# Performance work log

Hardware: AMD Instinct MI355X
Metric: run time of the kernel (lower is better)

Reference implementation:

```python
import jax, jax.numpy as jnp
import numpy as np

I, H, NH, A = 128, 2048, 2, 4   # input_size, hidden_size, n_hidden, alpha_dim
K = 2 * A * A                   # per-position theta entries
B = 8192


def make_masks():
    # MADE sequential-ordering masks, identical to DART.create_masks
    inp = np.arange(I)
    degrees = [inp] + [np.arange(H) % (I - 1) for _ in range(NH + 1)] + [np.arange(I) - 1]
    masks = [(d1[:, None] >= d0[None, :]).astype(np.float32)
             for d0, d1 in zip(degrees[:-1], degrees[1:])]
    # last mask repeated per theta entry: repeat(1, K).view(-1, H) == row-repeat
    masks[-1] = np.repeat(masks[-1], K, axis=0)
    return [jnp.asarray(m) for m in masks]


def setup_inputs() -> dict:
    key = jax.random.key(0)
    ks = jax.random.split(key, 5)
    x = jax.random.normal(ks[0], (B, I), dtype=jnp.float32)

    def lin(k, out_dim, in_dim):
        kw, kb = jax.random.split(k)
        s = 1.0 / np.sqrt(in_dim)
        W = jax.random.uniform(kw, (out_dim, in_dim), minval=-s, maxval=s, dtype=jnp.float32)
        b = jax.random.uniform(kb, (out_dim,), minval=-s, maxval=s, dtype=jnp.float32)
        return W, b

    W0, b0 = lin(ks[1], H, I)
    W1, b1 = lin(ks[2], H, H)
    W2, b2 = lin(ks[3], H, H)
    W3, b3 = lin(ks[4], I * K, H)
    return dict(x=x, W0=W0, b0=b0, W1=W1, b1=b1, W2=W2, b2=b2, W3=W3, b3=b3)


def logexpmm(a, b):
    # log-domain matmul: out[..., i, j] = logsumexp_k(a[..., i, k] + b[..., k, j])
    return jax.nn.logsumexp(a[..., :, :, None] + b[..., None, :, :], axis=-2)


def reference(x, W0, b0, W1, b1, W2, b2, W3, b3):
    m = make_masks()
    h = jax.nn.relu(x @ (m[0] * W0).T + b0)
    h = jax.nn.relu(h @ (m[1] * W1).T + b1)
    h = jax.nn.relu(h @ (m[2] * W2).T + b2)
    theta = (h @ (m[3] * W3).T + b3).reshape(-1, I, 2, A, A)
    mu, alpha = theta[:, :, 0], theta[:, :, 1]  # (B, I, A, A)

    LOG2PI = float(np.log(2.0 * np.pi))
    xe = x[:, :, None, None]
    # Normal(mu, exp(alpha)).log_prob(x) - log(alpha_dim)
    logp = (-0.5 * ((xe - mu) * jnp.exp(-alpha)) ** 2
            - alpha - 0.5 * LOG2PI - jnp.log(jnp.float32(A)))

    first = logp[:, 0, 0:1]        # (B, 1, A)
    last = logp[:, -1, :, 0:1]     # (B, A, 1)
    inner = jnp.swapaxes(logp[:, 1:-1], 0, 1)  # (I-2, B, A, A)

    def step(carry, mtx):
        return logexpmm(carry, mtx), None

    prod, _ = jax.lax.scan(step, inner[0], inner[1:])
    return logexpmm(first, logexpmm(prod, last))  # (B, 1, 1)
```

## Files before the change

### kernel.cpp

```cpp
#include <hip/hip_runtime.h>
#include <hip/hip_bf16.h>
#include <cstdint>
#include <cstddef>

#define AS1 __attribute__((address_space(1)))
#define AS3 __attribute__((address_space(3)))

typedef __bf16 bf16x8  __attribute__((ext_vector_type(8)));
typedef float  floatx4 __attribute__((ext_vector_type(4)));

__device__ __forceinline__ void load_lds16(const void* g, void* l) {
    __builtin_amdgcn_global_load_lds((AS1 void*)g, (AS3 void*)l, 16, 0, 0);
}

__device__ __forceinline__ float fexp2(float x) { return __builtin_amdgcn_exp2f(x); }
__device__ __forceinline__ float flog2(float x) { return __builtin_amdgcn_logf(x); }

#define LOG2E 1.4426950408889634f
#define LN2   0.6931471805599453f
#define C0K   2.3052328943245633f

__device__ __forceinline__ float logp2(float xv, float mu, float al) {
    float e = fexp2(-al * LOG2E);
    float z = (xv - mu) * e;
    return (-0.5f * z * z - al - C0K) * LOG2E;
}
__device__ __forceinline__ float lse4(float a0, float a1, float a2, float a3) {
    float mx = fmaxf(fmaxf(a0, a1), fmaxf(a2, a3));
    return mx + flog2(fexp2(a0 - mx) + fexp2(a1 - mx) +
                      fexp2(a2 - mx) + fexp2(a3 - mx));
}
__device__ __forceinline__ void lmm4(const float* Aa, const float* Bb, float* D) {
#pragma unroll
    for (int r = 0; r < 4; ++r)
#pragma unroll
        for (int c = 0; c < 4; ++c)
            D[r * 4 + c] = lse4(Aa[r * 4 + 0] + Bb[0 * 4 + c],
                                Aa[r * 4 + 1] + Bb[1 * 4 + c],
                                Aa[r * 4 + 2] + Bb[2 * 4 + c],
                                Aa[r * 4 + 3] + Bb[3 * 4 + c]);
}

__device__ __forceinline__ int resp_s(int p) {
    return p < 272 ? p / 17 : 16 + ((p - 272) >> 4);
}
__device__ __forceinline__ int invp_s(int p) {
    if (p < 272) { int d = p / 17; int r = p - d * 17;
                   return r < 16 ? d + r * 127 : 2032 + d; }
    int d = 16 + ((p - 272) >> 4); int j = (p - 272) & 15;
    return d + j * 127;
}
__device__ __forceinline__ int cnt_le(int D) {
    return D < 16 ? (D + 1) * 17 : 272 + ((D - 15) << 4);
}

__global__ __launch_bounds__(256)
void prep_all(const float* __restrict__ x,  const float* __restrict__ W0,
              const float* __restrict__ W1, const float* __restrict__ W2,
              const float* __restrict__ W3,
              __bf16* __restrict__ xb,  __bf16* __restrict__ w0m,
              __bf16* __restrict__ w1m, __bf16* __restrict__ w2m,
              __bf16* __restrict__ w3m)
{
    __shared__ float lds[2048];
    const int blk = blockIdx.x;
    const int tid = threadIdx.x;
    const int t8  = tid * 8;

    if (blk < 640) {
        bf16x8 o;
        if (blk < 512) {
            size_t base = (size_t)blk * 2048 + t8;
            floatx4 a = *(const floatx4*)(x + base);
            floatx4 b = *(const floatx4*)(x + base + 4);
#pragma unroll
            for (int j = 0; j < 4; ++j) { o[j] = (__bf16)a[j]; o[4 + j] = (__bf16)b[j]; }
            *(bf16x8*)(xb + base) = o;
        } else {
            long idx = (long)(blk - 512) * 2048 + t8;
            int p_n = (int)(idx >> 7);
            int c   = (int)(idx & 127);
            int dg  = resp_s(p_n);
            const float* s = W0 + (long)invp_s(p_n) * 128 + c;
            floatx4 a = *(const floatx4*)s;
            floatx4 b = *(const floatx4*)(s + 4);
#pragma unroll
            for (int j = 0; j < 8; ++j) {
                float v = j < 4 ? a[j] : b[j - 4];
                o[j] = (__bf16)((dg >= c + j) ? v : 0.0f);
            }
            *(bf16x8*)(w0m + idx) = o;
        }
        return;
    }

    const float* srow; __bf16* drow; int deg_n; bool strict;
    if (blk < 2688) {
        int p_n = blk - 640;
        srow = W1 + (size_t)invp_s(p_n) * 2048; drow = w1m + (size_t)p_n * 2048;
        deg_n = resp_s(p_n); strict = false;
    } else if (blk < 4736) {
        int p_n = blk - 2688;
        srow = W2 + (size_t)invp_s(p_n) * 2048; drow = w2m + (size_t)p_n * 2048;
        deg_n = resp_s(p_n); strict = false;
    } else {
        int n = blk - 4736;
        srow = W3 + (size_t)n * 2048; drow = w3m + (size_t)n * 2048;
        deg_n = n >> 5; strict = true;
    }
    floatx4 a = *(const floatx4*)(srow + t8);
    floatx4 b = *(const floatx4*)(srow + t8 + 4);
    *(floatx4*)&lds[t8]     = a;
    *(floatx4*)&lds[t8 + 4] = b;
    __syncthreads();
    bf16x8 o;
#pragma unroll
    for (int j = 0; j < 8; ++j) {
        int p = t8 + j;
        float v = lds[invp_s(p)];
        int dg = resp_s(p);
        bool keep = strict ? (deg_n > dg) : (deg_n >= dg);
        o[j] = (__bf16)(keep ? v : 0.0f);
    }
    *(bf16x8*)(drow + t8) = o;
}

template <bool RELU, bool OBF16, bool TLAYOUT, bool PERMBIAS, int LMODE>
__global__ __launch_bounds__(256, 4)
void gemm_bt(const __bf16* __restrict__ A, const __bf16* __restrict__ Bw,
             const float* __restrict__ bias, void* __restrict__ Cout,
             int N, int K)
{
    __shared__ __align__(16) __bf16 lsA[128 * 64];
    __shared__ __align__(16) __bf16 lsB[128 * 64];
    const int tid  = threadIdx.x;
    const int wave = tid >> 6;
    const int lane = tid & 63;
    const int bm = blockIdx.x;
    const int bn = (gridDim.y - 1) - blockIdx.y;
    const int wm = wave >> 1, wn = wave & 1;

    const int r8 = lane >> 3;
    const int cb = (lane & 7) ^ r8;
    const __bf16* gsrc[8];
    __bf16* ldst[8];
#pragma unroll
    for (int t = 0; t < 8; ++t) {
        int j = wave * 8 + t;
        if (j < 16) {
            int row = bm * 128 + j * 8 + r8;
            gsrc[t] = A + (size_t)row * K + cb * 8;
            ldst[t] = lsA + j * 512;
        } else {
            int jj = j - 16;
            int row = bn * 128 + jj * 8 + r8;
            gsrc[t] = Bw + (size_t)row * K + cb * 8;
            ldst[t] = lsB + jj * 512;
        }
    }

    const int fr  = lane & 15;
    const int ks  = lane >> 4;
    const int sx  = fr & 7;
    const int sl0 = ((ks)     ^ sx) * 8;
    const int sl1 = ((4 + ks) ^ sx) * 8;
    const __bf16* arow[4];
    const __bf16* brow[4];
#pragma unroll
    for (int i = 0; i < 4; ++i) {
        arow[i] = lsA + (wm * 64 + i * 16 + fr) * 64;
        brow[i] = lsB + (wn * 64 + i * 16 + fr) * 64;
    }

    floatx4 acc[4][4];
    const floatx4 vzero = {0.f, 0.f, 0.f, 0.f};
#pragma unroll
    for (int mi = 0; mi < 4; ++mi)
#pragma unroll
        for (int ni = 0; ni < 4; ++ni) acc[mi][ni] = vzero;

    const int nk = K >> 6;
    int limit;
    if (LMODE == 0)      limit = (cnt_le(resp_s(bn * 128 + 127)) + 63) >> 6;
    else if (LMODE == 1) { int D = 4 * bn + 2; if (D > 126) D = 126;
                           limit = (cnt_le(D) + 63) >> 6; }
    else                 limit = (resp_s(bn * 128 + 127) + 64) >> 6;
    if (limit > nk) limit = nk;

    for (int it = 0; it < limit; ++it) {
        const int kt = it << 6;
        __syncthreads();
#pragma unroll
        for (int t = 0; t < 8; ++t)
            load_lds16((const void*)(gsrc[t] + kt), (void*)ldst[t]);
        __syncthreads();
        bf16x8 af[4], bf[4];
#pragma unroll
        for (int i = 0; i < 4; ++i) af[i] = *(const bf16x8*)(arow[i] + sl0);
#pragma unroll
        for (int i = 0; i < 4; ++i) bf[i] = *(const bf16x8*)(brow[i] + sl0);
#pragma unroll
        for (int mi = 0; mi < 4; ++mi)
#pragma unroll
            for (int ni = 0; ni < 4; ++ni)
                acc[mi][ni] = __builtin_amdgcn_mfma_f32_16x16x32_bf16(
                    af[mi], bf[ni], acc[mi][ni], 0, 0, 0);
#pragma unroll
        for (int i = 0; i < 4; ++i) af[i] = *(const bf16x8*)(arow[i] + sl1);
#pragma unroll
        for (int i = 0; i < 4; ++i) bf[i] = *(const bf16x8*)(brow[i] + sl1);
#pragma unroll
        for (int mi = 0; mi < 4; ++mi)
#pragma unroll
            for (int ni = 0; ni < 4; ++ni)
                acc[mi][ni] = __builtin_amdgcn_mfma_f32_16x16x32_bf16(
                    af[mi], bf[ni], acc[mi][ni], 0, 0, 0);
    }

    const int cn  = lane & 15;
    const int cr4 = (lane >> 4) * 4;
#pragma unroll
    for (int ni = 0; ni < 4; ++ni) {
        int col = bn * 128 + wn * 64 + ni * 16 + cn;
        float bv = bias[PERMBIAS ? invp_s(col) : col];
#pragma unroll
        for (int mi = 0; mi < 4; ++mi) {
            int row0 = bm * 128 + wm * 64 + mi * 16 + cr4;
#pragma unroll
            for (int q = 0; q < 4; ++q) {
                float v = acc[mi][ni][q] + bv;
                if (RELU) v = fmaxf(v, 0.f);
                if (TLAYOUT) {
                    size_t addr = (size_t)(bm * 2 + wm) * ((size_t)N * 64)
                                + (size_t)(col >> 5) * 2048
                                + (size_t)(mi * 16 + cr4 + q) * 32 + (col & 31);
                    ((__bf16*)Cout)[addr] = (__bf16)v;
                } else if (OBF16) {
                    ((__bf16*)Cout)[(size_t)(row0 + q) * N + col] = (__bf16)v;
                } else {
                    ((float*)Cout)[(size_t)(row0 + q) * N + col] = v;
                }
            }
        }
    }
}

#define CFENCE() asm volatile("" ::: "memory")
#define BARX()  do { CFENCE(); __builtin_amdgcn_s_barrier(); CFENCE(); } while (0)
#define WVM2()  asm volatile("s_waitcnt vmcnt(2)" ::: "memory")
#define WVM0()  asm volatile("s_waitcnt vmcnt(0)" ::: "memory")
#define WLGK()  asm volatile("s_waitcnt lgkmcnt(0)" ::: "memory")

template <bool RELU, bool OBF16, bool TLAYOUT, bool PERMBIAS, int LMODE>
__global__ __launch_bounds__(512)
void gemm8p(const __bf16* __restrict__ A, const __bf16* __restrict__ Bw,
            const float* __restrict__ bias, void* __restrict__ Cout,
            int N, int K)
{
    __shared__ __align__(16) __bf16 ls[2 * 24576];
    const int tid  = threadIdx.x;
    const int wave = tid >> 6;
    const int lane = tid & 63;
    const int bm = blockIdx.x;
    const int bn = (gridDim.y - 1) - blockIdx.y;
    const int wm = wave >> 1, wn = wave & 1;

    const int l8 = lane >> 3;
    const int cb = (lane & 7) ^ l8;
    const __bf16* gA[2][2];  int dA[2][2];
    const __bf16* gB[2];     int dB[2];
#pragma unroll
    for (int h = 0; h < 2; ++h)
#pragma unroll
        for (int s = 0; s < 2; ++s) {
            int rt = h * 128 + wave * 16 + s * 8;
            gA[h][s] = A + (size_t)(bm * 256 + rt + l8) * K + cb * 8;
            dA[h][s] = rt * 64;
        }
#pragma unroll
    for (int s = 0; s < 2; ++s) {
        int rt = wave * 16 + s * 8;
        gB[s] = Bw + (size_t)(bn * 128 + rt + l8) * K + cb * 8;
        dB[s] = 16384 + rt * 64;
    }

#define STG_A(buf, kt) do { \
    load_lds16((const void*)(gA[0][0] + (kt)), (void*)(ls + (buf)*24576 + dA[0][0])); \
    load_lds16((const void*)(gA[0][1] + (kt)), (void*)(ls + (buf)*24576 + dA[0][1])); \
    load_lds16((const void*)(gA[1][0] + (kt)), (void*)(ls + (buf)*24576 + dA[1][0])); \
    load_lds16((const void*)(gA[1][1] + (kt)), (void*)(ls + (buf)*24576 + dA[1][1])); } while (0)
#define STG_B(buf, kt) do { \
    load_lds16((const void*)(gB[0] + (kt)), (void*)(ls + (buf)*24576 + dB[0])); \
    load_lds16((const void*)(gB[1] + (kt)), (void*)(ls + (buf)*24576 + dB[1])); } while (0)

    const int fr  = lane & 15;
    const int ks  = lane >> 4;
    const int sx  = fr & 7;
    const int sl0 = ((ks)     ^ sx) * 8;
    const int sl1 = ((4 + ks) ^ sx) * 8;
    int aoff[4], boff[4];
#pragma unroll
    for (int i = 0; i < 4; ++i) {
        aoff[i] = (wm * 64 + i * 16 + fr) * 64;
        boff[i] = 16384 + (wn * 64 + i * 16 + fr) * 64;
    }

    floatx4 acc[4][4];
    const floatx4 vzero = {0.f, 0.f, 0.f, 0.f};
#pragma unroll
    for (int mi = 0; mi < 4; ++mi)
#pragma unroll
        for (int ni = 0; ni < 4; ++ni) acc[mi][ni] = vzero;

    bf16x8 bfr[4][2], afr[2][2];

#define DSRD_B(buf) do { \
    _Pragma("unroll") \
    for (int ni = 0; ni < 4; ++ni) { \
        bfr[ni][0] = *(const bf16x8*)(ls + (buf)*24576 + boff[ni] + sl0); \
        bfr[ni][1] = *(const bf16x8*)(ls + (buf)*24576 + boff[ni] + sl1); } } while (0)
#define DSRD_A(buf, q) do { \
    _Pragma("unroll") \
    for (int j = 0; j < 2; ++j) { \
        afr[j][0] = *(const bf16x8*)(ls + (buf)*24576 + aoff[2*(q)+j] + sl0); \
        afr[j][1] = *(const bf16x8*)(ls + (buf)*24576 + aoff[2*(q)+j] + sl1); } } while (0)
#define MFMA16(q) do { \
    __builtin_amdgcn_s_setprio(1); \
    _Pragma("unroll") \
    for (int j = 0; j < 2; ++j) \
    _Pragma("unroll") \
    for (int ni = 0; ni < 4; ++ni) { \
        acc[2*(q)+j][ni] = __builtin_amdgcn_mfma_f32_16x16x32_bf16( \
            afr[j][0], bfr[ni][0], acc[2*(q)+j][ni], 0, 0, 0); \
        acc[2*(q)+j][ni] = __builtin_amdgcn_mfma_f32_16x16x32_bf16( \
            afr[j][1], bfr[ni][1], acc[2*(q)+j][ni], 0, 0, 0); } \
    __builtin_amdgcn_s_setprio(0); } while (0)

    const int nk = K >> 6;
    int limit;
    if (LMODE == 0)      limit = (cnt_le(resp_s(bn * 128 + 127)) + 63) >> 6;
    else if (LMODE == 1) { int D = 4 * bn + 2; if (D > 126) D = 126;
                           limit = (cnt_le(D) + 63) >> 6; }
    else                 limit = (resp_s(bn * 128 + 127) + 64) >> 6;
    if (limit > nk) limit = nk;
    const int NT = limit;

    STG_B(0, 0);
    STG_A(0, 0);
    if (NT > 1) { STG_B(1, 64); WVM2(); } else { WVM0(); }
    BARX();

    for (int t = 0; ; t += 2) {
        const int kt1 = (t + 1) << 6, kt2 = (t + 2) << 6, kt3 = (t + 3) << 6;
        const bool has1 = t + 1 < NT, has2 = t + 2 < NT, has3 = t + 3 < NT;

        DSRD_B(0);
        DSRD_A(0, 0);
        if (has1) STG_A(1, kt1);
        BARX(); WLGK();
        MFMA16(0);
        BARX();

        DSRD_A(0, 1);
        if (has2) STG_B(0, kt2);
        BARX(); WLGK();
        MFMA16(1);
        if (!has1) break;
        if (has2) WVM2(); else WVM0();
        BARX();

        DSRD_B(1);
        DSRD_A(1, 0);
        if (has2) STG_A(0, kt2);
        BARX(); WLGK();
        MFMA16(0);
        BARX();

        DSRD_A(1, 1);
        if (has3) STG_B(1, kt3);
        BARX(); WLGK();
        MFMA16(1);
        if (!has2) break;
        if (has3) WVM2(); else WVM0();
        BARX();
    }

    const int cn  = lane & 15;
    const int cr4 = (lane >> 4) * 4;
#pragma unroll
    for (int ni = 0; ni < 4; ++ni) {
        int col = bn * 128 + wn * 64 + ni * 16 + cn;
        float bv = bias[PERMBIAS ? invp_s(col) : col];
#pragma unroll
        for (int mi = 0; mi < 4; ++mi) {
            int row0 = bm * 256 + wm * 64 + mi * 16 + cr4;
#pragma unroll
            for (int q = 0; q < 4; ++q) {
                float v = acc[mi][ni][q] + bv;
                if (RELU) v = fmaxf(v, 0.f);
                if (TLAYOUT) {
                    size_t addr = (size_t)(bm * 4 + wm) * ((size_t)N * 64)
                                + (size_t)(col >> 5) * 2048
                                + (size_t)(mi * 16 + cr4 + q) * 32 + (col & 31);
                    ((__bf16*)Cout)[addr] = (__bf16)v;
                } else if (OBF16) {
                    ((__bf16*)Cout)[(size_t)(row0 + q) * N + col] = (__bf16)v;
                } else {
                    ((float*)Cout)[(size_t)(row0 + q) * N + col] = v;
                }
            }
        }
    }
#undef STG_A
#undef STG_B
#undef DSRD_B
#undef DSRD_A
#undef MFMA16
}

__global__ __launch_bounds__(576)
void chain_all(const __bf16* __restrict__ th2,
               const float* __restrict__ x,
               float* __restrict__ out)
{
    __shared__ float xs[32 * 129];
    __shared__ float Pl[32 * 306];
    const int tid = threadIdx.x;
    const int blk = blockIdx.x;

    for (int idx = tid; idx < 4096; idx += 576) {
        int bl = idx >> 7, i = idx & 127;
        xs[bl * 129 + i] = x[(size_t)blk * 4096 + idx];
    }
    __syncthreads();

    const int s  = tid >> 5;
    const int bl = tid & 31;
    const int b64 = (blk & 1) * 32 + bl;
    const __bf16* tb = th2 + (size_t)(blk >> 1) * 262144 + (size_t)b64 * 32;

    {
        const int i0 = 1 + s * 7;
        const __bf16* tp = tb + (size_t)i0 * 2048;
        float M[4][4];
#pragma unroll
        for (int r = 0; r < 4; ++r)
#pragma unroll
            for (int c = 0; c < 4; ++c) M[r][c] = (r == c) ? 0.f : -1e30f;

        for (int ii = 0; ii < 7; ++ii) {
            bf16x8 v0 = *(const bf16x8*)(tp);
            bf16x8 v1 = *(const bf16x8*)(tp + 8);
            bf16x8 v2 = *(const bf16x8*)(tp + 16);
            bf16x8 v3 = *(const bf16x8*)(tp + 24);
            float mu[16], al[16];
#pragma unroll
            for (int j = 0; j < 8; ++j) {
                mu[j] = (float)v0[j]; mu[8 + j] = (float)v1[j];
                al[j] = (float)v2[j]; al[8 + j] = (float)v3[j];
            }
            float xv = xs[bl * 129 + i0 + ii];
            tp += 2048;
            float lp[16];
#pragma unroll
            for (int j = 0; j < 16; ++j) lp[j] = logp2(xv, mu[j], al[j]);
            float Mn[4][4];
#pragma unroll
            for (int r = 0; r < 4; ++r)
#pragma unroll
                for (int c = 0; c < 4; ++c)
                    Mn[r][c] = lse4(M[r][0] + lp[0 + c], M[r][1] + lp[4 + c],
                                    M[r][2] + lp[8 + c], M[r][3] + lp[12 + c]);
#pragma unroll
            for (int r = 0; r < 4; ++r)
#pragma unroll
                for (int c = 0; c < 4; ++c) M[r][c] = Mn[r][c];
        }
        float* pb = Pl + bl * 306 + s * 17;
#pragma unroll
        for (int r = 0; r < 4; ++r)
#pragma unroll
            for (int c = 0; c < 4; ++c) pb[r * 4 + c] = M[r][c];
    }
    __syncthreads();

    float Q[16];
    if (tid < 288) {
        const float* base = Pl + bl * 306;
        lmm4(base + (2 * s) * 17, base + (2 * s + 1) * 17, Q);
    }
    __syncthreads();
    if (tid < 288) {
        float* dst = Pl + bl * 306 + s * 17;
#pragma unroll
        for (int e = 0; e < 16; ++e) dst[e] = Q[e];
    }
    __syncthreads();

    if (tid < 32) {
        const float* base = Pl + tid * 306;
        float M[16], T[16];
#pragma unroll
        for (int e = 0; e < 16; ++e) M[e] = base[e];
#pragma unroll
        for (int j = 1; j < 9; ++j) {
            lmm4(M, base + j * 17, T);
#pragma unroll
            for (int e = 0; e < 16; ++e) M[e] = T[e];
        }
        const int bb64 = (blk & 1) * 32 + tid;
        const __bf16* tbb = th2 + (size_t)(blk >> 1) * 262144 + (size_t)bb64 * 32;
        float x0 = xs[tid * 129 + 0];
        float xl = xs[tid * 129 + 127];
        float last[4], t4[4], f4[4];
#pragma unroll
        for (int c = 0; c < 4; ++c)
            last[c] = logp2(xl, (float)tbb[(size_t)127 * 2048 + c * 4],
                                (float)tbb[(size_t)127 * 2048 + 16 + c * 4]);
#pragma unroll
        for (int r = 0; r < 4; ++r)
            t4[r] = lse4(M[r * 4 + 0] + last[0], M[r * 4 + 1] + last[1],
                         M[r * 4 + 2] + last[2], M[r * 4 + 3] + last[3]);
#pragma unroll
        for (int r = 0; r < 4; ++r)
            f4[r] = logp2(x0, (float)tbb[r], (float)tbb[16 + r]);
        out[blk * 32 + tid] = LN2 * lse4(f4[0] + t4[0], f4[1] + t4[1],
                                         f4[2] + t4[2], f4[3] + t4[3]);
    }
}

extern "C" void kernel_launch(void* const* d_in, const int* in_sizes, int n_in,
                              void* d_out, int out_size, void* d_ws, size_t ws_size,
                              hipStream_t stream)
{
    (void)in_sizes; (void)n_in; (void)out_size; (void)ws_size;
    const float* x  = (const float*)d_in[0];
    const float* W0 = (const float*)d_in[1];
    const float* b0 = (const float*)d_in[2];
    const float* W1 = (const float*)d_in[3];
    const float* b1 = (const float*)d_in[4];
    const float* W2 = (const float*)d_in[5];
    const float* b2 = (const float*)d_in[6];
    const float* W3 = (const float*)d_in[7];
    const float* b3 = (const float*)d_in[8];

    char* ws = (char*)d_ws;
    const size_t MB = 1024 * 1024;
    __bf16* h2  = (__bf16*)(ws + 0);
    __bf16* xb  = (__bf16*)(ws + 32 * MB);
    __bf16* w0m = (__bf16*)(ws + 34 * MB);
    __bf16* w1m = (__bf16*)(ws + 35 * MB);
    __bf16* w2m = (__bf16*)(ws + 43 * MB);
    __bf16* th  = (__bf16*)(ws + 0);
    __bf16* w3m = (__bf16*)(ws + 64 * MB);
    __bf16* h1  = (__bf16*)(ws + 80 * MB);
    __bf16* h3  = h1;

    prep_all<<<8832, 256, 0, stream>>>(x, W0, W1, W2, W3, xb, w0m, w1m, w2m, w3m);

    gemm_bt<true, true, false, true, 2><<<dim3(64, 16), 256, 0, stream>>>(
        xb, w0m, b0, h1, 2048, 128);
    gemm8p<true, true, false, true, 0><<<dim3(32, 16), 512, 0, stream>>>(
        h1, w1m, b1, h2, 2048, 2048);
    gemm8p<true, true, false, true, 0><<<dim3(32, 16), 512, 0, stream>>>(
        h2, w2m, b2, h3, 2048, 2048);
    gemm_bt<false, false, true, false, 1><<<dim3(64, 32), 256, 0, stream>>>(
        h3, w3m, b3, th, 4096, 2048);

    chain_all<<<256, 576, 0, stream>>>(th, x, (float*)d_out);
}
```

Baseline: 314.4 us.

## Fuse W1/W2/W3 mask-permute prep into first-layer GEMM launch

The single prep kernel is split in two. The x and W0 conversion stays in its own small launch. The masked, permuted W1/W2/W3 preparation moves into the same grid as the first-layer GEMM (blocks 0–1023 do the GEMM, the rest do weight prep), so the bandwidth-bound weight conversion can run alongside the short K=128 GEMM instead of before it. The gemm_bt body is factored into a device function, and the unused TLAYOUT path is removed from gemm8p. This keeps the launch count the same but overlaps the two stages, at the risk of GEMM and prep blocks competing for the same resources.

```diff
diff --git a/kernel.cpp b/kernel.cpp
--- a/kernel.cpp
+++ b/kernel.cpp
@@ -55,89 +55,46 @@
 }
 
 __global__ __launch_bounds__(256)
-void prep_all(const float* __restrict__ x,  const float* __restrict__ W0,
-              const float* __restrict__ W1, const float* __restrict__ W2,
-              const float* __restrict__ W3,
-              __bf16* __restrict__ xb,  __bf16* __restrict__ w0m,
-              __bf16* __restrict__ w1m, __bf16* __restrict__ w2m,
-              __bf16* __restrict__ w3m)
-{
-    __shared__ float lds[2048];
+void prep_xw0(const float* __restrict__ x, const float* __restrict__ W0,
+              __bf16* __restrict__ xb, __bf16* __restrict__ w0m)
+{
     const int blk = blockIdx.x;
     const int tid = threadIdx.x;
     const int t8  = tid * 8;
-
-    if (blk < 640) {
-        bf16x8 o;
-        if (blk < 512) {
-            size_t base = (size_t)blk * 2048 + t8;
-            floatx4 a = *(const floatx4*)(x + base);
-            floatx4 b = *(const floatx4*)(x + base + 4);
-#pragma unroll
-            for (int j = 0; j < 4; ++j) { o[j] = (__bf16)a[j]; o[4 + j] = (__bf16)b[j]; }
-            *(bf16x8*)(xb + base) = o;
-        } else {
-            long idx = (long)(blk - 512) * 2048 + t8;
-            int p_n = (int)(idx >> 7);
-            int c   = (int)(idx & 127);
-            int dg  = resp_s(p_n);
-            const float* s = W0 + (long)invp_s(p_n) * 128 + c;
-            floatx4 a = *(const floatx4*)s;
-            floatx4 b = *(const floatx4*)(s + 4);
-#pragma unroll
-            for (int j = 0; j < 8; ++j) {
-                float v = j < 4 ? a[j] : b[j - 4];
-                o[j] = (__bf16)((dg >= c + j) ? v : 0.0f);
-            }
-            *(bf16x8*)(w0m + idx) = o;
-        }
-        return;
-    }
-
-    const float* srow; __bf16* drow; int deg_n; bool strict;
-    if (blk < 2688) {
-        int p_n = blk - 640;
-        srow = W1 + (size_t)invp_s(p_n) * 2048; drow = w1m + (size_t)p_n * 2048;
-        deg_n = resp_s(p_n); strict = false;
-    } else if (blk < 4736) {
-        int p_n = blk - 2688;
-        srow = W2 + (size_t)invp_s(p_n) * 2048; drow = w2m + (size_t)p_n * 2048;
-        deg_n = resp_s(p_n); strict = false;
+    bf16x8 o;
+    if (blk < 512) {
+        size_t base = (size_t)blk * 2048 + t8;
+        floatx4 a = *(const floatx4*)(x + base);
+        floatx4 b = *(const floatx4*)(x + base + 4);
+#pragma unroll
+        for (int j = 0; j < 4; ++j) { o[j] = (__bf16)a[j]; o[4 + j] = (__bf16)b[j]; }
+        *(bf16x8*)(xb + base) = o;
     } else {
-        int n = blk - 4736;
-        srow = W3 + (size_t)n * 2048; drow = w3m + (size_t)n * 2048;
-        deg_n = n >> 5; strict = true;
-    }
-    floatx4 a = *(const floatx4*)(srow + t8);
-    floatx4 b = *(const floatx4*)(srow + t8 + 4);
-    *(floatx4*)&lds[t8]     = a;
-    *(floatx4*)&lds[t8 + 4] = b;
-    __syncthreads();
-    bf16x8 o;
-#pragma unroll
-    for (int j = 0; j < 8; ++j) {
-        int p = t8 + j;
-        float v = lds[invp_s(p)];
-        int dg = resp_s(p);
-        bool keep = strict ? (deg_n > dg) : (deg_n >= dg);
-        o[j] = (__bf16)(keep ? v : 0.0f);
-    }
-    *(bf16x8*)(drow + t8) = o;
+        long idx = (long)(blk - 512) * 2048 + t8;
+        int p_n = (int)(idx >> 7);
+        int c   = (int)(idx & 127);
+        int dg  = resp_s(p_n);
+        const float* s = W0 + (long)invp_s(p_n) * 128 + c;
+        floatx4 a = *(const floatx4*)s;
+        floatx4 b = *(const floatx4*)(s + 4);
+#pragma unroll
+        for (int j = 0; j < 8; ++j) {
+            float v = j < 4 ? a[j] : b[j - 4];
+            o[j] = (__bf16)((dg >= c + j) ? v : 0.0f);
+        }
+        *(bf16x8*)(w0m + idx) = o;
+    }
 }
 
 template <bool RELU, bool OBF16, bool TLAYOUT, bool PERMBIAS, int LMODE>
-__global__ __launch_bounds__(256, 4)
-void gemm_bt(const __bf16* __restrict__ A, const __bf16* __restrict__ Bw,
-             const float* __restrict__ bias, void* __restrict__ Cout,
-             int N, int K)
-{
-    __shared__ __align__(16) __bf16 lsA[128 * 64];
-    __shared__ __align__(16) __bf16 lsB[128 * 64];
-    const int tid  = threadIdx.x;
+__device__ __forceinline__
+void gemm_bt_body(const __bf16* __restrict__ A, const __bf16* __restrict__ Bw,
+                  const float* __restrict__ bias, void* __restrict__ Cout,
+                  int N, int K, int bm, int bn, int tid,
+                  __bf16* lsA, __bf16* lsB)
+{
     const int wave = tid >> 6;
     const int lane = tid & 63;
-    const int bm = blockIdx.x;
-    const int bn = (gridDim.y - 1) - blockIdx.y;
     const int wm = wave >> 1, wn = wave & 1;
 
     const int r8 = lane >> 3;
@@ -245,13 +202,81 @@
     }
 }
 
+template <bool RELU, bool OBF16, bool TLAYOUT, bool PERMBIAS, int LMODE>
+__global__ __launch_bounds__(256, 4)
+void gemm_bt(const __bf16* __restrict__ A, const __bf16* __restrict__ Bw,
+             const float* __restrict__ bias, void* __restrict__ Cout,
+             int N, int K)
+{
+    __shared__ __align__(16) __bf16 ls[2 * 8192];
+    const int bm = blockIdx.x;
+    const int bn = (gridDim.y - 1) - blockIdx.y;
+    gemm_bt_body<RELU, OBF16, TLAYOUT, PERMBIAS, LMODE>(
+        A, Bw, bias, Cout, N, K, bm, bn, threadIdx.x, ls, ls + 8192);
+}
+
+__global__ __launch_bounds__(256, 4)
+void g0_prep(const __bf16* __restrict__ xb, const __bf16* __restrict__ w0m,
+             const float* __restrict__ b0, __bf16* __restrict__ h1,
+             const float* __restrict__ W1, const float* __restrict__ W2,
+             const float* __restrict__ W3,
+             __bf16* __restrict__ w1m, __bf16* __restrict__ w2m,
+             __bf16* __restrict__ w3m)
+{
+    __shared__ __align__(16) __bf16 ls[2 * 8192];
+    const int id  = blockIdx.x;
+    const int tid = threadIdx.x;
+
+    if (id < 1024) {
+        int bm = id & 63;
+        int bn = 15 - (id >> 6);
+        gemm_bt_body<true, true, false, true, 2>(
+            xb, w0m, b0, h1, 2048, 128, bm, bn, tid, ls, ls + 8192);
+        return;
+    }
+
+    const int blk = id - 384;
+    const int t8  = tid * 8;
+    float* lds = (float*)ls;
+
+    const float* srow; __bf16* drow; int deg_n; bool strict;
+    if (blk < 2688) {
+        int p_n = blk - 640;
+        srow = W1 + (size_t)invp_s(p_n) * 2048; drow = w1m + (size_t)p_n * 2048;
+        deg_n = resp_s(p_n); strict = false;
+    } else if (blk < 4736) {
+        int p_n = blk - 2688;
+        srow = W2 + (size_t)invp_s(p_n) * 2048; drow = w2m + (size_t)p_n * 2048;
+        deg_n = resp_s(p_n); strict = false;
+    } else {
+        int n = blk - 4736;
+        srow = W3 + (size_t)n * 2048; drow = w3m + (size_t)n * 2048;
+        deg_n = n >> 5; strict = true;
+    }
+    floatx4 a = *(const floatx4*)(srow + t8);
+    floatx4 b = *(const floatx4*)(srow + t8 + 4);
+    *(floatx4*)&lds[t8]     = a;
+    *(floatx4*)&lds[t8 + 4] = b;
+    __syncthreads();
+    bf16x8 o;
+#pragma unroll
+    for (int j = 0; j < 8; ++j) {
+        int p = t8 + j;
+        float v = lds[invp_s(p)];
+        int dg = resp_s(p);
+        bool keep = strict ? (deg_n > dg) : (deg_n >= dg);
+        o[j] = (__bf16)(keep ? v : 0.0f);
+    }
+    *(bf16x8*)(drow + t8) = o;
+}
+
 #define CFENCE() asm volatile("" ::: "memory")
 #define BARX()  do { CFENCE(); __builtin_amdgcn_s_barrier(); CFENCE(); } while (0)
 #define WVM2()  asm volatile("s_waitcnt vmcnt(2)" ::: "memory")
 #define WVM0()  asm volatile("s_waitcnt vmcnt(0)" ::: "memory")
 #define WLGK()  asm volatile("s_waitcnt lgkmcnt(0)" ::: "memory")
 
-template <bool RELU, bool OBF16, bool TLAYOUT, bool PERMBIAS, int LMODE>
+template <bool RELU, bool OBF16, bool PERMBIAS, int LMODE>
 __global__ __launch_bounds__(512)
 void gemm8p(const __bf16* __restrict__ A, const __bf16* __restrict__ Bw,
             const float* __restrict__ bias, void* __restrict__ Cout,
@@ -398,12 +423,7 @@
             for (int q = 0; q < 4; ++q) {
                 float v = acc[mi][ni][q] + bv;
                 if (RELU) v = fmaxf(v, 0.f);
-                if (TLAYOUT) {
-                    size_t addr = (size_t)(bm * 4 + wm) * ((size_t)N * 64)
-                                + (size_t)(col >> 5) * 2048
-                                + (size_t)(mi * 16 + cr4 + q) * 32 + (col & 31);
-                    ((__bf16*)Cout)[addr] = (__bf16)v;
-                } else if (OBF16) {
+                if (OBF16) {
                     ((__bf16*)Cout)[(size_t)(row0 + q) * N + col] = (__bf16)v;
                 } else {
                     ((float*)Cout)[(size_t)(row0 + q) * N + col] = v;
@@ -556,16 +576,14 @@
     __bf16* h1  = (__bf16*)(ws + 80 * MB);
     __bf16* h3  = h1;
 
-    prep_all<<<8832, 256, 0, stream>>>(x, W0, W1, W2, W3, xb, w0m, w1m, w2m, w3m);
-
-    gemm_bt<true, true, false, true, 2><<<dim3(64, 16), 256, 0, stream>>>(
-        xb, w0m, b0, h1, 2048, 128);
-    gemm8p<true, true, false, true, 0><<<dim3(32, 16), 512, 0, stream>>>(
+    prep_xw0<<<640, 256, 0, stream>>>(x, W0, xb, w0m);
+    g0_prep<<<9216, 256, 0, stream>>>(xb, w0m, b0, h1, W1, W2, W3,
+                                      w1m, w2m, w3m);
+    gemm8p<true, true, true, 0><<<dim3(32, 16), 512, 0, stream>>>(
         h1, w1m, b1, h2, 2048, 2048);
-    gemm8p<true, true, false, true, 0><<<dim3(32, 16), 512, 0, stream>>>(
+    gemm8p<true, true, true, 0><<<dim3(32, 16), 512, 0, stream>>>(
         h2, w2m, b2, h3, 2048, 2048);
     gemm_bt<false, false, true, false, 1><<<dim3(64, 32), 256, 0, stream>>>(
         h3, w3m, b3, th, 4096, 2048);
-
     chain_all<<<256, 576, 0, stream>>>(th, x, (float*)d_out);
 }
```

Result: no change. 320.3 us (+1.9%).
